# Kernel tuning notes

Measured on AMD Instinct MI355X. Metric: run time of the kernel, lower is better.

The kernel has to match this reference:

```python
import jax, jax.numpy as jnp
import numpy as np

N_NODES = 10000
N_EDGES = 160000
HIDDEN = 256
HEADS = 8
LN_EPS = 1e-5


def setup_inputs() -> dict:
    key = jax.random.key(0)
    ks = jax.random.split(key, 8)
    s = 1.0 / np.sqrt(HIDDEN)
    return {
        "node_embeddings": jax.random.normal(ks[0], (1, N_NODES, HIDDEN), jnp.float32),
        "edge_index": jax.random.randint(ks[1], (2, N_EDGES), 0, N_NODES, dtype=jnp.int32),
        "Wq": jax.random.normal(ks[2], (HIDDEN, HIDDEN), jnp.float32) * s,
        "Wk": jax.random.normal(ks[3], (HIDDEN, HIDDEN), jnp.float32) * s,
        "Wv": jax.random.normal(ks[4], (HIDDEN, HIDDEN), jnp.float32) * s,
        "Wo": jax.random.normal(ks[5], (HIDDEN, HIDDEN), jnp.float32) * s,
        "ln_gamma": jnp.ones((HIDDEN,), jnp.float32),
        "ln_beta": jnp.zeros((HIDDEN,), jnp.float32),
    }


def reference(node_embeddings, edge_index, Wq, Wk, Wv, Wo, ln_gamma, ln_beta):
    B, N, Dm = node_embeddings.shape
    H = HEADS
    hd = Dm // H
    scale = 1.0 / np.sqrt(hd)

    def heads(x):  # [B,N,Dm] -> [B,H,N,hd]
        return x.reshape(B, N, H, hd).transpose(0, 2, 1, 3)

    Q = heads(node_embeddings @ Wq)
    K = heads(node_embeddings @ Wk)
    V = heads(node_embeddings @ Wv)

    src, dst = edge_index[0], edge_index[1]
    Qe = Q[:, :, src, :]           # [B,H,E,hd]
    Ke = K[:, :, dst, :]
    Ve = V[:, :, dst, :]

    scores = jnp.einsum('bhed,bhed->bhe', Qe, Ke) * scale   # [B,H,E]
    s_t = scores.transpose(2, 0, 1)                          # [E,B,H]
    smax = jax.ops.segment_max(s_t, src, num_segments=N)    # [N,B,H]
    ex = jnp.exp(s_t - smax[src])                            # [E,B,H]
    denom = jax.ops.segment_sum(ex, src, num_segments=N)    # [N,B,H]
    attn = ex / denom[src]                                   # scatter-softmax weights

    wV = attn[..., None] * Ve.transpose(2, 0, 1, 3)          # [E,B,H,hd]
    agg = jax.ops.segment_sum(wV, src, num_segments=N)      # [N,B,H,hd]
    attn_out = agg.transpose(1, 0, 2, 3).reshape(B, N, Dm)   # [B,N,Dm]

    out = attn_out @ Wo
    x = out + node_embeddings
    mu = jnp.mean(x, axis=-1, keepdims=True)
    var = jnp.mean((x - mu) ** 2, axis=-1, keepdims=True)
    return (x - mu) * jax.lax.rsqrt(var + LN_EPS) * ln_gamma + ln_beta
```

## Files before the change

kernel.cpp:

```cpp
#include <hip/hip_runtime.h>

#define NN 10000
#define NE 160000
#define DM 256
#define CAP 96
#define LN_EPSF 1e-5f
#define SCALEF 0.17677669529663687f

typedef unsigned short u16;
typedef __attribute__((ext_vector_type(4))) u16 u16x4;
typedef __attribute__((ext_vector_type(8))) u16 u16x8;
typedef __attribute__((ext_vector_type(4))) float f32x4;
typedef __attribute__((ext_vector_type(8))) short short8;

__device__ __forceinline__ float b2f(u16 u) { return __uint_as_float(((unsigned)u) << 16); }
__device__ __forceinline__ u16 f2b(float f) {
    unsigned u = __float_as_uint(f);
    return (u16)((u + 0x7fffu + ((u >> 16) & 1u)) >> 16);
}
__device__ __forceinline__ int clampi(int v) { return v < 0 ? 0 : (v >= NN ? NN - 1 : v); }

__global__ void k_fill_zero_f32(float* __restrict__ o, int n) {
    int i = blockIdx.x * 256 + threadIdx.x;
    if (i < n) o[i] = 0.f;
}

#define UPD(mm, ss, AA, kv, p) do {                  \
    float nm_ = fmaxf(mm, p);                        \
    float al_ = __expf(mm - nm_);                    \
    float pe_ = __expf(p - nm_);                     \
    ss = ss * al_ + pe_;                             \
    AA[0] = AA[0] * al_ + pe_ * b2f(kv[4]);          \
    AA[1] = AA[1] * al_ + pe_ * b2f(kv[5]);          \
    AA[2] = AA[2] * al_ + pe_ * b2f(kv[6]);          \
    AA[3] = AA[3] * al_ + pe_ * b2f(kv[7]);          \
    mm = nm_;                                        \
} while (0)

__global__ void k_prep(const float* __restrict__ Wq, const float* __restrict__ Wk,
                       const float* __restrict__ Wv, const float* __restrict__ Wo,
                       u16* __restrict__ Wt, int* __restrict__ cnt) {
    int id = blockIdx.x * 256 + threadIdx.x;
    if (id < NN) cnt[id] = 0;
    int m = id >> 16;
    int rc = id & 65535;
    int r = rc >> 8, c = rc & 255;
    const float* W = (m == 0) ? Wq : (m == 1) ? Wk : (m == 2) ? Wv : Wo;
    Wt[m * 65536 + c * 256 + r] = f2b(W[r * 256 + c]);
}

__global__ __launch_bounds__(256) void k_qkv_bucket(const float* __restrict__ X, const u16* __restrict__ Wt,
                                                    u16* __restrict__ Q, u16* __restrict__ KV,
                                                    const int* __restrict__ EI, int* __restrict__ cnt,
                                                    int* __restrict__ buck) {
    constexpr int ALS = 264;
    __shared__ u16 AtL[32 * ALS];
    if (blockIdx.y == 3) {
        int e0 = blockIdx.x * 512 + threadIdx.x;
#pragma unroll
        for (int h = 0; h < 2; h++) {
            int e = e0 + h * 256;
            if (e < NE) {
                int s = clampi(EI[e]);
                int slot = atomicAdd(&cnt[s], 1);
                if (slot < CAP) buck[s * CAP + slot] = clampi(EI[NE + e]);
            }
        }
        return;
    }
    const int t = threadIdx.x;
    const int w = t >> 6, l = t & 63, quad = l >> 4, m16 = l & 15;
    const int mat = blockIdx.y;
    const u16* Wm = Wt + mat * 65536;
    const int node0 = blockIdx.x * 32;
    {
        const int arow = t >> 3, ac32 = (t & 7) * 32;
        const int anode = node0 + arow;
#pragma unroll
        for (int j = 0; j < 4; j++) {
            u16x8 av = {0, 0, 0, 0, 0, 0, 0, 0};
            if (anode < NN) {
                const float* xp = X + (size_t)anode * DM + ac32 + j * 8;
                f32x4 a0 = *(const f32x4*)(xp);
                f32x4 a1 = *(const f32x4*)(xp + 4);
                av[0] = f2b(a0[0]); av[1] = f2b(a0[1]); av[2] = f2b(a0[2]); av[3] = f2b(a0[3]);
                av[4] = f2b(a1[0]); av[5] = f2b(a1[1]); av[6] = f2b(a1[2]); av[7] = f2b(a1[3]);
            }
            *(u16x8*)(AtL + arow * ALS + ac32 + j * 8) = av;
        }
    }
    __syncthreads();
    f32x4 acc[2][4];
#pragma unroll
    for (int i = 0; i < 2; i++)
#pragma unroll
        for (int j = 0; j < 4; j++) acc[i][j] = (f32x4){0.f, 0.f, 0.f, 0.f};
    for (int k0 = 0; k0 < DM; k0 += 32) {
        short8 a[2], b[4];
#pragma unroll
        for (int rt = 0; rt < 2; rt++)
            a[rt] = *(const short8*)(AtL + (rt * 16 + m16) * ALS + k0 + quad * 8);
#pragma unroll
        for (int ct = 0; ct < 4; ct++)
            b[ct] = *(const short8*)(Wm + (size_t)(w * 64 + ct * 16 + m16) * DM + k0 + quad * 8);
#pragma unroll
        for (int rt = 0; rt < 2; rt++)
#pragma unroll
            for (int ct = 0; ct < 4; ct++)
                acc[rt][ct] = __builtin_amdgcn_mfma_f32_16x16x32_bf16(a[rt], b[ct], acc[rt][ct], 0, 0, 0);
    }
#pragma unroll
    for (int rt = 0; rt < 2; rt++) {
#pragma unroll
        for (int ct = 0; ct < 4; ct++) {
            int col = w * 64 + ct * 16 + m16;
#pragma unroll
            for (int r = 0; r < 4; r++) {
                int node = node0 + rt * 16 + quad * 4 + r;
                if (node < NN) {
                    u16 v = f2b(acc[rt][ct][r]);
                    if (mat == 0) Q[(size_t)node * DM + col] = v;
                    else KV[(size_t)node * 512 + (col >> 2) * 8 + (col & 3) + ((mat == 2) ? 4 : 0)] = v;
                }
            }
        }
    }
}

__global__ __launch_bounds__(256) void k_edge(const u16* __restrict__ Q, const u16* __restrict__ KV,
                                              const int* __restrict__ cnt, const int* __restrict__ buck,
                                              u16* __restrict__ attn) {
    const int t = threadIdx.x;
    const int w = t >> 6, l = t & 63;
    const int node = blockIdx.x * 4 + w;
    const int d0 = l * 4;
    int deg = cnt[node];
    if (deg > CAP) deg = CAP;
    const int* bl = buck + node * CAP;
    u16x4 q4 = *(const u16x4*)(Q + (size_t)node * DM + d0);
    float qf0 = b2f(q4[0]) * SCALEF, qf1 = b2f(q4[1]) * SCALEF;
    float qf2 = b2f(q4[2]) * SCALEF, qf3 = b2f(q4[3]) * SCALEF;
    float mm[8], ss[8];
    f32x4 AA[8];
#pragma unroll
    for (int j = 0; j < 8; j++) {
        mm[j] = -3.0e38f;
        ss[j] = 0.f;
        AA[j] = (f32x4){0.f, 0.f, 0.f, 0.f};
    }
    int i = 0;
    int deg8 = deg & ~7;
    for (; i < deg8; i += 8) {
        int4 ea = *(const int4*)(bl + i);
        int4 eb = *(const int4*)(bl + i + 4);
        int dst[8] = {ea.x, ea.y, ea.z, ea.w, eb.x, eb.y, eb.z, eb.w};
        u16x8 kv[8];
#pragma unroll
        for (int j = 0; j < 8; j++)
            kv[j] = *(const u16x8*)(KV + (size_t)dst[j] * 512 + l * 8);
        float p[8];
#pragma unroll
        for (int j = 0; j < 8; j++)
            p[j] = qf0 * b2f(kv[j][0]) + qf1 * b2f(kv[j][1]) + qf2 * b2f(kv[j][2]) + qf3 * b2f(kv[j][3]);
#pragma unroll
        for (int j = 0; j < 8; j++) p[j] += __shfl_xor(p[j], 1, 64);
#pragma unroll
        for (int j = 0; j < 8; j++) p[j] += __shfl_xor(p[j], 2, 64);
#pragma unroll
        for (int j = 0; j < 8; j++) p[j] += __shfl_xor(p[j], 4, 64);
#pragma unroll
        for (int j = 0; j < 8; j++) UPD(mm[j], ss[j], AA[j], kv[j], p[j]);
    }
    for (; i < deg; ++i) {
        int dst = bl[i];
        u16x8 kv = *(const u16x8*)(KV + (size_t)dst * 512 + l * 8);
        float p = qf0 * b2f(kv[0]) + qf1 * b2f(kv[1]) + qf2 * b2f(kv[2]) + qf3 * b2f(kv[3]);
        p += __shfl_xor(p, 1, 64);
        p += __shfl_xor(p, 2, 64);
        p += __shfl_xor(p, 4, 64);
        UPD(mm[0], ss[0], AA[0], kv, p);
    }
    float nm = mm[0];
#pragma unroll
    for (int j = 1; j < 8; j++) nm = fmaxf(nm, mm[j]);
    float S = 0.f, O0 = 0.f, O1 = 0.f, O2 = 0.f, O3 = 0.f;
#pragma unroll
    for (int j = 0; j < 8; j++) {
        float wj = __expf(mm[j] - nm);
        S += ss[j] * wj;
        O0 += AA[j][0] * wj;
        O1 += AA[j][1] * wj;
        O2 += AA[j][2] * wj;
        O3 += AA[j][3] * wj;
    }
    float inv = (S > 0.f) ? 1.f / S : 0.f;
    u16x4 o;
    o[0] = f2b(O0 * inv);
    o[1] = f2b(O1 * inv);
    o[2] = f2b(O2 * inv);
    o[3] = f2b(O3 * inv);
    *(u16x4*)(attn + (size_t)node * DM + d0) = o;
}

__global__ __launch_bounds__(256) void k_gemm_out_ln(const u16* __restrict__ In, const u16* __restrict__ WoT,
                                                     const float* __restrict__ X, const float* __restrict__ g,
                                                     const float* __restrict__ b, float* __restrict__ out) {
    constexpr int ALS = 264;
    __shared__ u16 AtL[32 * ALS];
    __shared__ float gbuf[256], bbuf[256];
    __shared__ float redS[4][32], redQ[4][32], muS[32], rsS[32];
    const int t = threadIdx.x;
    gbuf[t] = g[t];
    bbuf[t] = b[t];
    const int w = t >> 6, l = t & 63, quad = l >> 4, m16 = l & 15;
    const int node0 = blockIdx.x * 32;
    {
        const int arow = t >> 3, ac32 = (t & 7) * 32;
        const int anode = node0 + arow;
#pragma unroll
        for (int j = 0; j < 4; j++) {
            u16x8 av = {0, 0, 0, 0, 0, 0, 0, 0};
            if (anode < NN) av = *(const u16x8*)(In + (size_t)anode * DM + ac32 + j * 8);
            *(u16x8*)(AtL + arow * ALS + ac32 + j * 8) = av;
        }
    }
    __syncthreads();
    f32x4 acc[2][4];
#pragma unroll
    for (int i = 0; i < 2; i++)
#pragma unroll
        for (int j = 0; j < 4; j++) acc[i][j] = (f32x4){0.f, 0.f, 0.f, 0.f};
    for (int k0 = 0; k0 < DM; k0 += 32) {
        short8 a[2], bf[4];
#pragma unroll
        for (int rt = 0; rt < 2; rt++)
            a[rt] = *(const short8*)(AtL + (rt * 16 + m16) * ALS + k0 + quad * 8);
#pragma unroll
        for (int ct = 0; ct < 4; ct++)
            bf[ct] = *(const short8*)(WoT + (size_t)(w * 64 + ct * 16 + m16) * DM + k0 + quad * 8);
#pragma unroll
        for (int rt = 0; rt < 2; rt++)
#pragma unroll
            for (int ct = 0; ct < 4; ct++)
                acc[rt][ct] = __builtin_amdgcn_mfma_f32_16x16x32_bf16(a[rt], bf[ct], acc[rt][ct], 0, 0, 0);
    }
#pragma unroll
    for (int rt = 0; rt < 2; rt++)
#pragma unroll
        for (int ct = 0; ct < 4; ct++) {
            int col = w * 64 + ct * 16 + m16;
#pragma unroll
            for (int r = 0; r < 4; r++) {
                int node = node0 + rt * 16 + quad * 4 + r;
                float x = (node < NN) ? X[(size_t)node * DM + col] : 0.f;
                acc[rt][ct][r] += x;
            }
        }
#pragma unroll
    for (int rt = 0; rt < 2; rt++) {
#pragma unroll
        for (int r = 0; r < 4; r++) {
            float p1 = acc[rt][0][r] + acc[rt][1][r] + acc[rt][2][r] + acc[rt][3][r];
            float p2 = acc[rt][0][r] * acc[rt][0][r] + acc[rt][1][r] * acc[rt][1][r] +
                       acc[rt][2][r] * acc[rt][2][r] + acc[rt][3][r] * acc[rt][3][r];
#pragma unroll
            for (int o = 1; o < 16; o <<= 1) {
                p1 += __shfl_xor(p1, o, 64);
                p2 += __shfl_xor(p2, o, 64);
            }
            if (m16 == 0) {
                int row = rt * 16 + quad * 4 + r;
                redS[w][row] = p1;
                redQ[w][row] = p2;
            }
        }
    }
    __syncthreads();
    if (t < 32) {
        float s1t = redS[0][t] + redS[1][t] + redS[2][t] + redS[3][t];
        float s2t = redQ[0][t] + redQ[1][t] + redQ[2][t] + redQ[3][t];
        float mm = s1t * (1.f / DM);
        float var = s2t * (1.f / DM) - mm * mm;
        muS[t] = mm;
        rsS[t] = rsqrtf(var + LN_EPSF);
    }
    __syncthreads();
#pragma unroll
    for (int rt = 0; rt < 2; rt++)
#pragma unroll
        for (int ct = 0; ct < 4; ct++) {
            int col = w * 64 + ct * 16 + m16;
#pragma unroll
            for (int r = 0; r < 4; r++) {
                int row = rt * 16 + quad * 4 + r;
                int node = node0 + row;
                if (node < NN)
                    out[(size_t)node * DM + col] = (acc[rt][ct][r] - muS[row]) * rsS[row] * gbuf[col] + bbuf[col];
            }
        }
}

extern "C" void kernel_launch(void* const* d_in, const int* in_sizes, int n_in,
                              void* d_out, int out_size, void* d_ws, size_t ws_size,
                              hipStream_t stream) {
    (void)in_sizes; (void)n_in;
    const float* X  = (const float*)d_in[0];
    const int*   EI = (const int*)d_in[1];
    const float* Wq = (const float*)d_in[2];
    const float* Wk = (const float*)d_in[3];
    const float* Wv = (const float*)d_in[4];
    const float* Wo = (const float*)d_in[5];
    const float* g  = (const float*)d_in[6];
    const float* be = (const float*)d_in[7];

    const size_t SWT  = (size_t)4 * 65536 * 2;
    const size_t SKV  = (size_t)NN * 512 * 2;
    const size_t SCNT = (size_t)NN * 4;
    const size_t SBK  = (size_t)NN * CAP * 4;
    const size_t SQB  = (size_t)NN * DM * 2;
    const size_t SAT  = (size_t)NN * DM * 2;
    const size_t need = SWT + SKV + SCNT + SBK + SQB + SAT;
    if (ws_size < need) {
        k_fill_zero_f32<<<(out_size + 255) / 256, 256, 0, stream>>>((float*)d_out, out_size);
        return;
    }
    char* p = (char*)d_ws;
    u16* Wt   = (u16*)p; p += SWT;
    u16* KVb  = (u16*)p; p += SKV;
    int* cnt  = (int*)p; p += SCNT;
    int* buck = (int*)p; p += SBK;
    u16* Qb   = (u16*)p; p += SQB;
    u16* attn = (u16*)p; p += SAT;

    k_prep<<<1024, 256, 0, stream>>>(Wq, Wk, Wv, Wo, Wt, cnt);
    k_qkv_bucket<<<dim3(313, 4), 256, 0, stream>>>(X, Wt, Qb, KVb, EI, cnt, buck);
    k_edge<<<NN / 4, 256, 0, stream>>>(Qb, KVb, cnt, buck, attn);
    k_gemm_out_ln<<<313, 256, 0, stream>>>(attn, Wt + 3 * 65536, X, g, be, (float*)d_out);
}
```

Baseline: 150.9 us.

## Split KV layout and process two edges per wave in edge kernel

The KV buffer changes from an interleaved K/V layout to separate contiguous K and V halves per node. In the edge kernel each half-wave of 32 lanes now handles a different edge with 8 dims per lane, and the two halves' online-softmax states are merged by a cross-half shuffle at the end; blocks shrink to 128 threads with two nodes each. The GEMM kernels also software-prefetch the next B fragment from global memory before issuing the current MFMAs. This aims to raise memory-level parallelism and cut shuffle and softmax overhead per edge, at the cost of more registers and a masked tail path.

Result: faster. 147.8 us (-2.0%).

```diff
diff --git a/kernel.cpp b/kernel.cpp
--- a/kernel.cpp
+++ b/kernel.cpp
@@ -24,18 +24,6 @@
     int i = blockIdx.x * 256 + threadIdx.x;
     if (i < n) o[i] = 0.f;
 }
-
-#define UPD(mm, ss, AA, kv, p) do {                  \
-    float nm_ = fmaxf(mm, p);                        \
-    float al_ = __expf(mm - nm_);                    \
-    float pe_ = __expf(p - nm_);                     \
-    ss = ss * al_ + pe_;                             \
-    AA[0] = AA[0] * al_ + pe_ * b2f(kv[4]);          \
-    AA[1] = AA[1] * al_ + pe_ * b2f(kv[5]);          \
-    AA[2] = AA[2] * al_ + pe_ * b2f(kv[6]);          \
-    AA[3] = AA[3] * al_ + pe_ * b2f(kv[7]);          \
-    mm = nm_;                                        \
-} while (0)
 
 __global__ void k_prep(const float* __restrict__ Wq, const float* __restrict__ Wk,
                        const float* __restrict__ Wv, const float* __restrict__ Wo,
@@ -95,19 +83,31 @@
     for (int i = 0; i < 2; i++)
 #pragma unroll
         for (int j = 0; j < 4; j++) acc[i][j] = (f32x4){0.f, 0.f, 0.f, 0.f};
+    short8 bc[4];
+#pragma unroll
+    for (int ct = 0; ct < 4; ct++)
+        bc[ct] = *(const short8*)(Wm + (size_t)(w * 64 + ct * 16 + m16) * DM + quad * 8);
+#pragma unroll
     for (int k0 = 0; k0 < DM; k0 += 32) {
-        short8 a[2], b[4];
+        short8 bn[4];
+        if (k0 + 32 < DM) {
+#pragma unroll
+            for (int ct = 0; ct < 4; ct++)
+                bn[ct] = *(const short8*)(Wm + (size_t)(w * 64 + ct * 16 + m16) * DM + (k0 + 32) + quad * 8);
+        }
+        short8 a[2];
 #pragma unroll
         for (int rt = 0; rt < 2; rt++)
             a[rt] = *(const short8*)(AtL + (rt * 16 + m16) * ALS + k0 + quad * 8);
 #pragma unroll
-        for (int ct = 0; ct < 4; ct++)
-            b[ct] = *(const short8*)(Wm + (size_t)(w * 64 + ct * 16 + m16) * DM + k0 + quad * 8);
-#pragma unroll
         for (int rt = 0; rt < 2; rt++)
 #pragma unroll
             for (int ct = 0; ct < 4; ct++)
-                acc[rt][ct] = __builtin_amdgcn_mfma_f32_16x16x32_bf16(a[rt], b[ct], acc[rt][ct], 0, 0, 0);
+                acc[rt][ct] = __builtin_amdgcn_mfma_f32_16x16x32_bf16(a[rt], bc[ct], acc[rt][ct], 0, 0, 0);
+        if (k0 + 32 < DM) {
+#pragma unroll
+            for (int ct = 0; ct < 4; ct++) bc[ct] = bn[ct];
+        }
     }
 #pragma unroll
     for (int rt = 0; rt < 2; rt++) {
@@ -120,86 +120,118 @@
                 if (node < NN) {
                     u16 v = f2b(acc[rt][ct][r]);
                     if (mat == 0) Q[(size_t)node * DM + col] = v;
-                    else KV[(size_t)node * 512 + (col >> 2) * 8 + (col & 3) + ((mat == 2) ? 4 : 0)] = v;
+                    else KV[(size_t)node * 512 + col + ((mat == 2) ? 256 : 0)] = v;
                 }
             }
         }
     }
 }
 
-__global__ __launch_bounds__(256) void k_edge(const u16* __restrict__ Q, const u16* __restrict__ KV,
+#define UPD8(mm, ss, AA, vv, p, msk) do {                 \
+    float nm_ = fmaxf(mm, p);                             \
+    float al_ = __expf(mm - nm_);                         \
+    float pe_ = __expf(p - nm_) * (msk);                  \
+    ss = ss * al_ + pe_;                                  \
+    _Pragma("unroll")                                     \
+    for (int d_ = 0; d_ < 8; d_++)                        \
+        AA[d_] = AA[d_] * al_ + pe_ * b2f(vv[d_]);        \
+    mm = nm_;                                             \
+} while (0)
+
+__global__ __launch_bounds__(128) void k_edge(const u16* __restrict__ Q, const u16* __restrict__ KV,
                                               const int* __restrict__ cnt, const int* __restrict__ buck,
                                               u16* __restrict__ attn) {
     const int t = threadIdx.x;
-    const int w = t >> 6, l = t & 63;
-    const int node = blockIdx.x * 4 + w;
-    const int d0 = l * 4;
+    const int wv = t >> 6, l = t & 63;
+    const int hl = l & 31, up = l >> 5;
+    const int node = blockIdx.x * 2 + wv;
     int deg = cnt[node];
     if (deg > CAP) deg = CAP;
     const int* bl = buck + node * CAP;
-    u16x4 q4 = *(const u16x4*)(Q + (size_t)node * DM + d0);
-    float qf0 = b2f(q4[0]) * SCALEF, qf1 = b2f(q4[1]) * SCALEF;
-    float qf2 = b2f(q4[2]) * SCALEF, qf3 = b2f(q4[3]) * SCALEF;
-    float mm[8], ss[8];
-    f32x4 AA[8];
-#pragma unroll
-    for (int j = 0; j < 8; j++) {
+    u16x8 q8 = *(const u16x8*)(Q + (size_t)node * DM + hl * 8);
+    float qf[8];
+#pragma unroll
+    for (int d = 0; d < 8; d++) qf[d] = b2f(q8[d]) * SCALEF;
+    float mm[4], ss[4], AA[4][8];
+#pragma unroll
+    for (int j = 0; j < 4; j++) {
         mm[j] = -3.0e38f;
         ss[j] = 0.f;
-        AA[j] = (f32x4){0.f, 0.f, 0.f, 0.f};
+#pragma unroll
+        for (int d = 0; d < 8; d++) AA[j][d] = 0.f;
     }
     int i = 0;
     int deg8 = deg & ~7;
     for (; i < deg8; i += 8) {
         int4 ea = *(const int4*)(bl + i);
         int4 eb = *(const int4*)(bl + i + 4);
-        int dst[8] = {ea.x, ea.y, ea.z, ea.w, eb.x, eb.y, eb.z, eb.w};
-        u16x8 kv[8];
-#pragma unroll
-        for (int j = 0; j < 8; j++)
-            kv[j] = *(const u16x8*)(KV + (size_t)dst[j] * 512 + l * 8);
-        float p[8];
-#pragma unroll
-        for (int j = 0; j < 8; j++)
-            p[j] = qf0 * b2f(kv[j][0]) + qf1 * b2f(kv[j][1]) + qf2 * b2f(kv[j][2]) + qf3 * b2f(kv[j][3]);
-#pragma unroll
-        for (int j = 0; j < 8; j++) p[j] += __shfl_xor(p[j], 1, 64);
-#pragma unroll
-        for (int j = 0; j < 8; j++) p[j] += __shfl_xor(p[j], 2, 64);
-#pragma unroll
-        for (int j = 0; j < 8; j++) p[j] += __shfl_xor(p[j], 4, 64);
-#pragma unroll
-        for (int j = 0; j < 8; j++) UPD(mm[j], ss[j], AA[j], kv[j], p[j]);
-    }
-    for (; i < deg; ++i) {
-        int dst = bl[i];
-        u16x8 kv = *(const u16x8*)(KV + (size_t)dst * 512 + l * 8);
-        float p = qf0 * b2f(kv[0]) + qf1 * b2f(kv[1]) + qf2 * b2f(kv[2]) + qf3 * b2f(kv[3]);
+        int dst[4];
+        dst[0] = up ? ea.y : ea.x;
+        dst[1] = up ? ea.w : ea.z;
+        dst[2] = up ? eb.y : eb.x;
+        dst[3] = up ? eb.w : eb.z;
+        u16x8 kk[4], vv[4];
+#pragma unroll
+        for (int j = 0; j < 4; j++) {
+            const u16* row = KV + (size_t)dst[j] * 512;
+            kk[j] = *(const u16x8*)(row + hl * 8);
+            vv[j] = *(const u16x8*)(row + 256 + hl * 8);
+        }
+        float p[4];
+#pragma unroll
+        for (int j = 0; j < 4; j++) {
+            float s = 0.f;
+#pragma unroll
+            for (int d = 0; d < 8; d++) s += qf[d] * b2f(kk[j][d]);
+            p[j] = s;
+        }
+#pragma unroll
+        for (int j = 0; j < 4; j++) p[j] += __shfl_xor(p[j], 1, 64);
+#pragma unroll
+        for (int j = 0; j < 4; j++) p[j] += __shfl_xor(p[j], 2, 64);
+#pragma unroll
+        for (int j = 0; j < 4; j++) UPD8(mm[j], ss[j], AA[j], vv[j], p[j], 1.0f);
+    }
+    for (; i < deg; i += 2) {
+        int jj = i + up;
+        float msk = (jj < deg) ? 1.f : 0.f;
+        int dst = bl[(jj < deg) ? jj : i];
+        const u16* row = KV + (size_t)dst * 512;
+        u16x8 kk = *(const u16x8*)(row + hl * 8);
+        u16x8 vv = *(const u16x8*)(row + 256 + hl * 8);
+        float p = 0.f;
+#pragma unroll
+        for (int d = 0; d < 8; d++) p += qf[d] * b2f(kk[d]);
         p += __shfl_xor(p, 1, 64);
         p += __shfl_xor(p, 2, 64);
-        p += __shfl_xor(p, 4, 64);
-        UPD(mm[0], ss[0], AA[0], kv, p);
-    }
-    float nm = mm[0];
-#pragma unroll
-    for (int j = 1; j < 8; j++) nm = fmaxf(nm, mm[j]);
-    float S = 0.f, O0 = 0.f, O1 = 0.f, O2 = 0.f, O3 = 0.f;
-#pragma unroll
-    for (int j = 0; j < 8; j++) {
+        UPD8(mm[0], ss[0], AA[0], vv, p, msk);
+    }
+    float nm = fmaxf(fmaxf(mm[0], mm[1]), fmaxf(mm[2], mm[3]));
+    float S = 0.f, O[8];
+#pragma unroll
+    for (int d = 0; d < 8; d++) O[d] = 0.f;
+#pragma unroll
+    for (int j = 0; j < 4; j++) {
         float wj = __expf(mm[j] - nm);
         S += ss[j] * wj;
-        O0 += AA[j][0] * wj;
-        O1 += AA[j][1] * wj;
-        O2 += AA[j][2] * wj;
-        O3 += AA[j][3] * wj;
-    }
-    float inv = (S > 0.f) ? 1.f / S : 0.f;
-    u16x4 o;
-    o[0] = f2b(O0 * inv);
-    o[1] = f2b(O1 * inv);
-    o[2] = f2b(O2 * inv);
-    o[3] = f2b(O3 * inv);
-    *(u16x4*)(attn + (size_t)node * DM + d0) = o;
+#pragma unroll
+        for (int d = 0; d < 8; d++) O[d] += AA[j][d] * wj;
+    }
+    float om = __shfl_xor(nm, 32, 64);
+    float oS = __shfl_xor(S, 32, 64);
+    float oO[8];
+#pragma unroll
+    for (int d = 0; d < 8; d++) oO[d] = __shfl_xor(O[d], 32, 64);
+    float fm = fmaxf(nm, om);
+    float wa = __expf(nm - fm), wb = __expf(om - fm);
+    float S2 = S * wa + oS * wb;
+    float inv = (S2 > 0.f) ? 1.f / S2 : 0.f;
+    if (up == 0) {
+        u16x8 o;
+#pragma unroll
+        for (int d = 0; d < 8; d++) o[d] = f2b((O[d] * wa + oO[d] * wb) * inv);
+        *(u16x8*)(attn + (size_t)node * DM + hl * 8) = o;
+    }
 }
 
 __global__ __launch_bounds__(256) void k_gemm_out_ln(const u16* __restrict__ In, const u16* __restrict__ WoT,
@@ -230,19 +262,31 @@
     for (int i = 0; i < 2; i++)
 #pragma unroll
         for (int j = 0; j < 4; j++) acc[i][j] = (f32x4){0.f, 0.f, 0.f, 0.f};
+    short8 bc[4];
+#pragma unroll
+    for (int ct = 0; ct < 4; ct++)
+        bc[ct] = *(const short8*)(WoT + (size_t)(w * 64 + ct * 16 + m16) * DM + quad * 8);
+#pragma unroll
     for (int k0 = 0; k0 < DM; k0 += 32) {
-        short8 a[2], bf[4];
+        short8 bn[4];
+        if (k0 + 32 < DM) {
+#pragma unroll
+            for (int ct = 0; ct < 4; ct++)
+                bn[ct] = *(const short8*)(WoT + (size_t)(w * 64 + ct * 16 + m16) * DM + (k0 + 32) + quad * 8);
+        }
+        short8 a[2];
 #pragma unroll
         for (int rt = 0; rt < 2; rt++)
             a[rt] = *(const short8*)(AtL + (rt * 16 + m16) * ALS + k0 + quad * 8);
 #pragma unroll
-        for (int ct = 0; ct < 4; ct++)
-            bf[ct] = *(const short8*)(WoT + (size_t)(w * 64 + ct * 16 + m16) * DM + k0 + quad * 8);
-#pragma unroll
         for (int rt = 0; rt < 2; rt++)
 #pragma unroll
             for (int ct = 0; ct < 4; ct++)
-                acc[rt][ct] = __builtin_amdgcn_mfma_f32_16x16x32_bf16(a[rt], bf[ct], acc[rt][ct], 0, 0, 0);
+                acc[rt][ct] = __builtin_amdgcn_mfma_f32_16x16x32_bf16(a[rt], bc[ct], acc[rt][ct], 0, 0, 0);
+        if (k0 + 32 < DM) {
+#pragma unroll
+            for (int ct = 0; ct < 4; ct++) bc[ct] = bn[ct];
+        }
     }
 #pragma unroll
     for (int rt = 0; rt < 2; rt++)
@@ -279,9 +323,9 @@
     if (t < 32) {
         float s1t = redS[0][t] + redS[1][t] + redS[2][t] + redS[3][t];
         float s2t = redQ[0][t] + redQ[1][t] + redQ[2][t] + redQ[3][t];
-        float mm = s1t * (1.f / DM);
-        float var = s2t * (1.f / DM) - mm * mm;
-        muS[t] = mm;
+        float mmv = s1t * (1.f / DM);
+        float var = s2t * (1.f / DM) - mmv * mmv;
+        muS[t] = mmv;
         rsS[t] = rsqrtf(var + LN_EPSF);
     }
     __syncthreads();
@@ -334,6 +378,6 @@
 
     k_prep<<<1024, 256, 0, stream>>>(Wq, Wk, Wv, Wo, Wt, cnt);
     k_qkv_bucket<<<dim3(313, 4), 256, 0, stream>>>(X, Wt, Qb, KVb, EI, cnt, buck);
-    k_edge<<<NN / 4, 256, 0, stream>>>(Qb, KVb, cnt, buck, attn);
+    k_edge<<<NN / 2, 128, 0, stream>>>(Qb, KVb, cnt, buck, attn);
     k_gemm_out_ln<<<313, 256, 0, stream>>>(attn, Wt + 3 * 65536, X, g, be, (float*)d_out);
 }
```
